# Kernel tuning notes

Hardware: AMD Instinct MI355X
Metric: run time of the kernel (lower is better)

## Reference

```python
import jax, jax.numpy as jnp
import numpy as np

B, S, HID = 2, 2048, 2048
NH, NKV, HD = 16, 4, 128  # num_heads, num_kv_heads, head_dim; kqv_size = NH*HD = 2048
KV_DIM = NKV * HD  # 512


def setup_inputs() -> dict:
    key = jax.random.key(0)
    ks = jax.random.split(key, 7)
    sc = 0.02
    return {
        "hidden_states": jax.random.normal(ks[0], (B, S, HID), dtype=jnp.float32),
        "Wq": jax.random.normal(ks[1], (NH * HD, HID), dtype=jnp.float32) * sc,
        "Wk": jax.random.normal(ks[2], (KV_DIM, HID), dtype=jnp.float32) * sc,
        "Wv": jax.random.normal(ks[3], (KV_DIM, HID), dtype=jnp.float32) * sc,
        "Wo": jax.random.normal(ks[4], (HID, NH * HD), dtype=jnp.float32) * sc,
        "bo": jnp.zeros((HID,), dtype=jnp.float32),
    }


def reference(hidden_states, Wq, Wk, Wv, Wo, bo):
    b, s, _ = hidden_states.shape
    # projections (nn.Linear: x @ W.T), no bias on q/k/v
    q = (hidden_states @ Wq.T).reshape(b, s, NH, HD).transpose(0, 2, 1, 3)   # [B,NH,S,HD]
    k = (hidden_states @ Wk.T).reshape(b, s, NKV, HD).transpose(0, 2, 1, 3)  # [B,NKV,S,HD]
    v = (hidden_states @ Wv.T).reshape(b, s, NKV, HD).transpose(0, 2, 1, 3)
    # GQA: query head h uses kv head h // (NH // NKV)
    g = NH // NKV
    k_rep = jnp.repeat(k, g, axis=1)  # [B,NH,S,HD]
    v_rep = jnp.repeat(v, g, axis=1)
    # float32 upcast, NO 1/sqrt(d) scaling (GPT-Neo style)
    qf = q.astype(jnp.float32)
    kf = k_rep.astype(jnp.float32)
    scores = jnp.einsum("bhqd,bhkd->bhqk", qf, kf)  # [B,NH,S,S]
    causal = jnp.tril(jnp.ones((s, s), dtype=bool))[None, None]
    neg = jnp.finfo(scores.dtype).min
    scores = jnp.where(causal, scores, neg)
    attn = jax.nn.softmax(scores, axis=-1).astype(v.dtype)  # dropout p=0 (eval)
    out = jnp.einsum("bhqk,bhkd->bhqd", attn, v_rep)         # [B,NH,S,HD]
    out = out.transpose(0, 2, 1, 3).reshape(b, s, NH * HD)
    return out @ Wo.T + bo
```

## Files before the change

kernel.cpp:

```cpp
#include <hip/hip_runtime.h>

typedef _Float16 f16;
typedef __attribute__((ext_vector_type(4))) _Float16 f16x4;
typedef __attribute__((ext_vector_type(8))) _Float16 f16x8;
typedef __attribute__((ext_vector_type(4))) float f32x4;

#define NB 2
#define NS 2048
#define NHID 2048
#define N_H 16
#define N_KV 4
#define N_HD 128

__device__ __forceinline__ void gload16(void* lds, const void* g) {
  __builtin_amdgcn_global_load_lds(
      (const __attribute__((address_space(1))) unsigned int*)g,
      (__attribute__((address_space(3))) unsigned int*)lds, 16, 0, 0);
}

__global__ __launch_bounds__(256) void cvt_all(
    const float* __restrict__ hs, const float* __restrict__ Wq,
    const float* __restrict__ Wk, const float* __restrict__ Wv,
    const float* __restrict__ Wo, f16* __restrict__ Xh,
    f16* __restrict__ Wqkv, f16* __restrict__ Woh) {
  int i = blockIdx.x * 256 + threadIdx.x;
  const float* src;
  f16* dst;
  int j;
  if (i < 2097152)      { src = hs; dst = Xh;             j = i; }
  else if (i < 3145728) { src = Wq; dst = Wqkv;           j = i - 2097152; }
  else if (i < 3407872) { src = Wk; dst = Wqkv + 4194304; j = i - 3145728; }
  else if (i < 3670016) { src = Wv; dst = Wqkv + 5242880; j = i - 3407872; }
  else                  { src = Wo; dst = Woh;            j = i - 3670016; }
  const float4 v = reinterpret_cast<const float4*>(src)[j];
  f16x4 o = {(f16)v.x, (f16)v.y, (f16)v.z, (f16)v.w};
  reinterpret_cast<f16x4*>(dst)[j] = o;
}

__global__ __launch_bounds__(512, 2) void gemm_qkv(
    const f16* __restrict__ A, const f16* __restrict__ Bm,
    f16* __restrict__ q_out, f16* __restrict__ k_out, f16* __restrict__ vt_out) {
  constexpr int K = 2048;
  constexpr int NT = 32;
  __shared__ f16 lds[2][28672];
  const int t = threadIdx.x;
  const int l = t & 63, w = t >> 6;
  const int g = l >> 4, l15 = l & 15;
  const int wr = w >> 2, wc = w & 3;
  const int orig = blockIdx.x;
  const int x = orig & 7, loc = orig >> 3;
  const int mb = (x & 3) * 4 + (loc & 3);
  const int nb = (x >> 2) * 8 + (loc >> 2);
  const f16* Ab = A + (size_t)(mb * 256) * K;
  const f16* Bb = Bm + (size_t)(nb * 192) * K;

  const int rr = ((t >> 5) << 3) | (t & 7);
  const int cc = (t >> 3) & 3;
  const int dstw = w * 512;
  int srcB[3];
#pragma unroll
  for (int j = 0; j < 3; ++j) {
    int db0 = j * 4096 + t * 8;
    int h = (db0 >= 6144) ? 1 : 0;
    int u = (db0 - h * 6144) >> 3;
    int rowB = ((u >> 5) << 3) | (u & 7);
    int ccB = (u >> 3) & 3;
    srcB[j] = rowB * K + h * 32 + ccB * 8;
  }

  auto stageA = [&](int tile, int j) {
    int h = j >> 1, gi = j & 1;
    gload16(&lds[tile & 1][h * 8192 + gi * 4096 + dstw],
            Ab + (size_t)(gi * 128 + rr) * K + tile * 64 + h * 32 + cc * 8);
  };
  auto stageB = [&](int tile, int j) {
    gload16(&lds[tile & 1][16384 + j * 4096 + dstw],
            Bb + (size_t)srcB[j] + tile * 64);
  };

  const int fragoff = ((l15 >> 3) << 8) + (g << 6) + ((l15 & 7) << 3);
  f32x4 acc[8][3] = {};

#pragma unroll
  for (int j = 0; j < 3; ++j) stageB(0, j);
#pragma unroll
  for (int j = 0; j < 4; ++j) stageA(0, j);
#pragma unroll
  for (int j = 0; j < 3; ++j) stageB(1, j);
  asm volatile("s_waitcnt vmcnt(3)" ::: "memory");
  __builtin_amdgcn_s_barrier();

  f16x8 bf[3][2];
  for (int T = 0; T < NT; ++T) {
    const f16* buf = lds[T & 1];
#pragma unroll
    for (int q = 0; q < 4; ++q) {
      f16x8 af[2][2];
#pragma unroll
      for (int i = 0; i < 2; ++i)
#pragma unroll
        for (int ks = 0; ks < 2; ++ks)
          af[i][ks] = *reinterpret_cast<const f16x8*>(
              buf + ks * 8192 + (wr * 128 + (2 * q + i) * 16) * 32 + fragoff);
      if (q == 0) {
#pragma unroll
        for (int ni = 0; ni < 3; ++ni)
#pragma unroll
          for (int ks = 0; ks < 2; ++ks)
            bf[ni][ks] = *reinterpret_cast<const f16x8*>(
                buf + 16384 + ks * 6144 + (wc * 48 + ni * 16) * 32 + fragoff);
      }
      if (q == 0)      { if (T + 1 < NT) { stageA(T + 1, 0); stageA(T + 1, 1); } }
      else if (q == 1) { if (T + 1 < NT) { stageA(T + 1, 2); stageA(T + 1, 3); } }
      else if (q == 2) { if (T + 2 < NT) { stageB(T + 2, 0); stageB(T + 2, 1); } }
      else             { if (T + 2 < NT) { stageB(T + 2, 2); } }
      __builtin_amdgcn_s_barrier();
      asm volatile("s_waitcnt lgkmcnt(0)" ::: "memory");
      __builtin_amdgcn_sched_barrier(0);
      __builtin_amdgcn_s_setprio(1);
#pragma unroll
      for (int i = 0; i < 2; ++i)
#pragma unroll
        for (int ni = 0; ni < 3; ++ni)
#pragma unroll
          for (int ks = 0; ks < 2; ++ks)
            acc[2 * q + i][ni] = __builtin_amdgcn_mfma_f32_16x16x32_f16(
                af[i][ks], bf[ni][ks], acc[2 * q + i][ni], 0, 0, 0);
      __builtin_amdgcn_s_setprio(0);
      if (q == 3 && T + 1 < NT) {
        if (T + 2 < NT) asm volatile("s_waitcnt vmcnt(3)" ::: "memory");
        else            asm volatile("s_waitcnt vmcnt(0)" ::: "memory");
      }
      __builtin_amdgcn_s_barrier();
    }
  }

#pragma unroll
  for (int mi = 0; mi < 8; ++mi) {
    int m0 = mb * 256 + wr * 128 + mi * 16 + 4 * g;
    int b = m0 >> 11, s0 = m0 & (NS - 1);
#pragma unroll
    for (int ni = 0; ni < 3; ++ni) {
      int n = nb * 192 + wc * 48 + ni * 16 + l15;
      if (n < 2048) {
        int h = n >> 7, d = n & 127;
        f16* qp = q_out + (((size_t)(b * N_H + h)) * NS + s0) * N_HD + d;
#pragma unroll
        for (int r = 0; r < 4; ++r) qp[r * N_HD] = (f16)acc[mi][ni][r];
      } else if (n < 2560) {
        int n2 = n - 2048, kvh = n2 >> 7, d = n2 & 127;
        f16* kp = k_out + (((size_t)(b * N_KV + kvh)) * NS + s0) * N_HD + d;
#pragma unroll
        for (int r = 0; r < 4; ++r) kp[r * N_HD] = (f16)acc[mi][ni][r];
      } else {
        int n3 = n - 2560, kvh = n3 >> 7, d = n3 & 127;
        f16x4 o4 = {(f16)acc[mi][ni][0], (f16)acc[mi][ni][1],
                    (f16)acc[mi][ni][2], (f16)acc[mi][ni][3]};
        *reinterpret_cast<f16x4*>(
            vt_out + (((size_t)(b * N_KV + kvh)) * N_HD + d) * NS + s0) = o4;
      }
    }
  }
}

__global__ __launch_bounds__(512, 2) void gemm_out(
    const f16* __restrict__ A, const f16* __restrict__ Bm,
    float* __restrict__ f_out, const float* __restrict__ bias) {
  constexpr int K = 2048;
  constexpr int NT = 32;
  __shared__ f16 lds[2][24576];
  const int t = threadIdx.x;
  const int l = t & 63, w = t >> 6;
  const int g = l >> 4, l15 = l & 15;
  const int wr = w >> 2, wc = w & 3;
  const int orig = blockIdx.x;
  const int x = orig & 7, loc = orig >> 3;
  const int mb = (x & 3) * 8 + (loc & 7);
  const int nb = (x >> 2) * 4 + (loc >> 3);
  const f16* Ab = A + (size_t)(mb * 128) * K;
  const f16* Bb = Bm + (size_t)(nb * 256) * K;

  const int rr = ((t >> 5) << 3) | (t & 7);
  const int cc = (t >> 3) & 3;
  const int dstw = w * 512;

  auto stageA = [&](int tile, int h) {
    gload16(&lds[tile & 1][h * 4096 + dstw],
            Ab + (size_t)rr * K + tile * 64 + h * 32 + cc * 8);
  };
  auto stageB = [&](int tile, int j) {
    int h = j >> 1, gi = j & 1;
    gload16(&lds[tile & 1][8192 + h * 8192 + gi * 4096 + dstw],
            Bb + (size_t)(gi * 128 + rr) * K + tile * 64 + h * 32 + cc * 8);
  };

  const int fragoff = ((l15 >> 3) << 8) + (g << 6) + ((l15 & 7) << 3);
  f32x4 acc[4][4] = {};

  stageA(0, 0); stageA(0, 1);
#pragma unroll
  for (int j = 0; j < 4; ++j) stageB(0, j);
#pragma unroll
  for (int j = 0; j < 4; ++j) stageB(1, j);
  asm volatile("s_waitcnt vmcnt(4)" ::: "memory");
  __builtin_amdgcn_s_barrier();

  f16x8 bf[4][2];
  for (int T = 0; T < NT; ++T) {
    const f16* buf = lds[T & 1];
#pragma unroll
    for (int q = 0; q < 2; ++q) {
      f16x8 af[2][2];
#pragma unroll
      for (int i = 0; i < 2; ++i)
#pragma unroll
        for (int ks = 0; ks < 2; ++ks)
          af[i][ks] = *reinterpret_cast<const f16x8*>(
              buf + ks * 4096 + (wr * 64 + (2 * q + i) * 16) * 32 + fragoff);
      if (q == 0) {
#pragma unroll
        for (int ni = 0; ni < 4; ++ni)
#pragma unroll
          for (int ks = 0; ks < 2; ++ks)
            bf[ni][ks] = *reinterpret_cast<const f16x8*>(
                buf + 8192 + ks * 8192 + (wc * 64 + ni * 16) * 32 + fragoff);
      }
      if (q == 0) {
        if (T + 1 < NT) { stageA(T + 1, 0); stageA(T + 1, 1); }
      } else {
        if (T + 2 < NT) { stageB(T + 2, 0); stageB(T + 2, 1); stageB(T + 2, 2); stageB(T + 2, 3); }
      }
      __builtin_amdgcn_s_barrier();
      asm volatile("s_waitcnt lgkmcnt(0)" ::: "memory");
      __builtin_amdgcn_sched_barrier(0);
      __builtin_amdgcn_s_setprio(1);
#pragma unroll
      for (int i = 0; i < 2; ++i)
#pragma unroll
        for (int ni = 0; ni < 4; ++ni)
#pragma unroll
          for (int ks = 0; ks < 2; ++ks)
            acc[2 * q + i][ni] = __builtin_amdgcn_mfma_f32_16x16x32_f16(
                af[i][ks], bf[ni][ks], acc[2 * q + i][ni], 0, 0, 0);
      __builtin_amdgcn_s_setprio(0);
      if (q == 1 && T + 1 < NT) {
        if (T + 2 < NT) asm volatile("s_waitcnt vmcnt(4)" ::: "memory");
        else            asm volatile("s_waitcnt vmcnt(0)" ::: "memory");
      }
      __builtin_amdgcn_s_barrier();
    }
  }

#pragma unroll
  for (int mi = 0; mi < 4; ++mi) {
    int m0 = mb * 128 + wr * 64 + mi * 16 + 4 * g;
#pragma unroll
    for (int ni = 0; ni < 4; ++ni) {
      int n = nb * 256 + wc * 64 + ni * 16 + l15;
#pragma unroll
      for (int r = 0; r < 4; ++r)
        f_out[(size_t)(m0 + r) * NHID + n] = acc[mi][ni][r] + bias[n];
    }
  }
}

__device__ __forceinline__ void stage_kv(const f16* __restrict__ Kp,
                                         const f16* __restrict__ Vp,
                                         f16* Kl, f16* Vl, int kt, int w, int l) {
#pragma unroll
  for (int it = 0; it < 4; ++it) {
    int cb = (it * 4 + w) * 64;
    int c = cb + l;
    int krow = c >> 4, pch = c & 15;
    int sch = (pch & 8) | ((pch ^ krow) & 7);
    gload16(Kl + cb * 8, Kp + (size_t)(kt * 64 + krow) * N_HD + sch * 8);
  }
#pragma unroll
  for (int it = 0; it < 4; ++it) {
    int cb = (it * 4 + w) * 64;
    int c = cb + l;
    int drow = c >> 3, pch = c & 7;
    int sch = (pch ^ drow) & 7;
    gload16(Vl + cb * 8, Vp + (size_t)drow * NS + kt * 64 + sch * 8);
  }
}

__device__ __forceinline__ void attn_step(
    const f16x8* qf, f32x4* oacc, float* mrow, float* lrow, int q0, int kt,
    const f16* Kl, const f16* Vl, f16* Pw, int g, int l15, bool diag) {
  f32x4 sacc[4];
#pragma unroll
  for (int nt = 0; nt < 4; ++nt) {
    f32x4 z = {0.f, 0.f, 0.f, 0.f};
#pragma unroll
    for (int ks = 0; ks < 4; ++ks) {
      int kr = nt * 16 + l15;
      int ch = ks * 4 + g;
      int sw = (ch & 8) | ((ch ^ kr) & 7);
      f16x8 kf = *reinterpret_cast<const f16x8*>(Kl + kr * 128 + sw * 8);
      z = __builtin_amdgcn_mfma_f32_16x16x32_f16(qf[ks], kf, z, 0, 0, 0);
    }
    sacc[nt] = z;
  }

  float p[4][4];
#pragma unroll
  for (int r = 0; r < 4; ++r) {
    int qg = q0 + r;
    float m = -3.0e38f;
#pragma unroll
    for (int nt = 0; nt < 4; ++nt) {
      float sv = sacc[nt][r];
      if (diag) {
        int kg = kt * 64 + nt * 16 + l15;
        if (kg > qg) sv = -3.0e38f;
      }
      p[nt][r] = sv;
      m = fmaxf(m, sv);
    }
#pragma unroll
    for (int off = 8; off >= 1; off >>= 1) m = fmaxf(m, __shfl_xor(m, off));
    float m2 = fmaxf(mrow[r], m);
    float alpha = __builtin_amdgcn_exp2f(mrow[r] - m2);
    mrow[r] = m2;
    lrow[r] *= alpha;
#pragma unroll
    for (int nt = 0; nt < 4; ++nt)
      p[nt][r] = __builtin_amdgcn_exp2f(p[nt][r] - m2);
#pragma unroll
    for (int dt = 0; dt < 8; ++dt) oacc[dt][r] *= alpha;
  }

#pragma unroll
  for (int nt = 0; nt < 4; ++nt)
#pragma unroll
    for (int r = 0; r < 4; ++r) {
      int ql = 4 * g + r;
      int kp = nt * 16 + l15;
      int ch = kp >> 3;
      int idx = ql * 64 + (ch ^ (ql & 7)) * 8 + (kp & 7);
      Pw[idx] = (f16)p[nt][r];
    }
  asm volatile("s_waitcnt lgkmcnt(0)" ::: "memory");
  __builtin_amdgcn_sched_barrier(0);

  f16x8 pa[2];
#pragma unroll
  for (int ks2 = 0; ks2 < 2; ++ks2) {
    int ch = ks2 * 4 + g;
    pa[ks2] = *reinterpret_cast<const f16x8*>(&Pw[l15 * 64 + (ch ^ (l15 & 7)) * 8]);
  }
  const f16x8 ones = {(f16)1.f, (f16)1.f, (f16)1.f, (f16)1.f,
                      (f16)1.f, (f16)1.f, (f16)1.f, (f16)1.f};
  f32x4 lacc = {0.f, 0.f, 0.f, 0.f};
#pragma unroll
  for (int ks2 = 0; ks2 < 2; ++ks2)
    lacc = __builtin_amdgcn_mfma_f32_16x16x32_f16(pa[ks2], ones, lacc, 0, 0, 0);
#pragma unroll
  for (int dt = 0; dt < 8; ++dt)
#pragma unroll
    for (int ks2 = 0; ks2 < 2; ++ks2) {
      int d = dt * 16 + l15;
      int ch = ks2 * 4 + g;
      f16x8 vf = *reinterpret_cast<const f16x8*>(Vl + d * 64 + (ch ^ (d & 7)) * 8);
      oacc[dt] = __builtin_amdgcn_mfma_f32_16x16x32_f16(pa[ks2], vf, oacc[dt], 0, 0, 0);
    }
#pragma unroll
  for (int r = 0; r < 4; ++r) lrow[r] += lacc[r];
}

__global__ __launch_bounds__(256, 2) void attn_kernel(
    const f16* __restrict__ Q, const f16* __restrict__ K,
    const f16* __restrict__ Vt, f16* __restrict__ O) {
  __shared__ f16 Klds[2][64 * 128];
  __shared__ f16 Vlds[2][128 * 64];
  __shared__ f16 Plds[4][16 * 64];
  const int t = threadIdx.x, l = t & 63, w = t >> 6;
  const int g = l >> 4, l15 = l & 15;
  const int orig = blockIdx.x;
  const int x = orig & 7, loc = orig >> 3;
  const int b = x >> 2, kvh = x & 3;
  const int h = kvh * 4 + (loc & 3);
  const int pi = loc >> 2;
  const int qtA = pi, qtB = 31 - pi;
  const f16* Qp = Q + ((size_t)(b * N_H + h)) * NS * N_HD;
  const f16* Kp = K + ((size_t)(b * N_KV + kvh)) * NS * N_HD;
  const f16* Vp = Vt + ((size_t)(b * N_KV + kvh)) * N_HD * NS;

  const f16 l2e = (f16)1.44269504f;
  f16x8 qfA[4], qfB[4];
  const int qrA = qtA * 64 + w * 16 + l15;
  const int qrB = qtB * 64 + w * 16 + l15;
#pragma unroll
  for (int ks = 0; ks < 4; ++ks) {
    qfA[ks] = *reinterpret_cast<const f16x8*>(Qp + (size_t)qrA * N_HD + ks * 32 + g * 8);
    qfB[ks] = *reinterpret_cast<const f16x8*>(Qp + (size_t)qrB * N_HD + ks * 32 + g * 8);
#pragma unroll
    for (int j = 0; j < 8; ++j) { qfA[ks][j] *= l2e; qfB[ks][j] *= l2e; }
  }

  f32x4 oA[8] = {}, oB[8] = {};
  float mA[4], lAr[4], mB[4], lBr[4];
#pragma unroll
  for (int r = 0; r < 4; ++r) {
    mA[r] = -3.0e38f; lAr[r] = 0.f;
    mB[r] = -3.0e38f; lBr[r] = 0.f;
  }
  const int q0A = qtA * 64 + w * 16 + 4 * g;
  const int q0B = qtB * 64 + w * 16 + 4 * g;

  const int nkt = qtB + 1;
  stage_kv(Kp, Vp, Klds[0], Vlds[0], 0, w, l);
  asm volatile("s_waitcnt vmcnt(0)" ::: "memory");
  __syncthreads();
  int cur = 0;
  for (int kt = 0; kt < nkt; ++kt) {
    if (kt + 1 < nkt)
      stage_kv(Kp, Vp, Klds[cur ^ 1], Vlds[cur ^ 1], kt + 1, w, l);
    attn_step(qfB, oB, mB, lBr, q0B, kt, Klds[cur], Vlds[cur], Plds[w], g, l15, kt == qtB);
    if (kt <= qtA)
      attn_step(qfA, oA, mA, lAr, q0A, kt, Klds[cur], Vlds[cur], Plds[w], g, l15, kt == qtA);
    asm volatile("s_waitcnt vmcnt(0)" ::: "memory");
    __syncthreads();
    cur ^= 1;
  }

#pragma unroll
  for (int r = 0; r < 4; ++r) {
    float invB = 1.0f / lBr[r];
    f16* orowB = O + (size_t)(b * NS + q0B + r) * NHID + h * N_HD;
#pragma unroll
    for (int dt = 0; dt < 8; ++dt) orowB[dt * 16 + l15] = (f16)(oB[dt][r] * invB);
    float invA = 1.0f / lAr[r];
    f16* orowA = O + (size_t)(b * NS + q0A + r) * NHID + h * N_HD;
#pragma unroll
    for (int dt = 0; dt < 8; ++dt) orowA[dt * 16 + l15] = (f16)(oA[dt][r] * invA);
  }
}

extern "C" void kernel_launch(void* const* d_in, const int* in_sizes, int n_in,
                              void* d_out, int out_size, void* d_ws, size_t ws_size,
                              hipStream_t stream) {
  const float* hs = (const float*)d_in[0];
  const float* Wq = (const float*)d_in[1];
  const float* Wk = (const float*)d_in[2];
  const float* Wv = (const float*)d_in[3];
  const float* Wo = (const float*)d_in[4];
  const float* bo = (const float*)d_in[5];
  float* out = (float*)d_out;

  char* ws = (char*)d_ws;
  f16* Xh   = (f16*)(ws);
  f16* Wqkv = (f16*)(ws + 16777216);
  f16* Woh  = (f16*)(ws + 29360128);
  f16* Qb   = (f16*)(ws + 37748736);
  f16* Kb   = (f16*)(ws + 54525952);
  f16* Vtb  = (f16*)(ws + 62914560);
  f16* Ob   = Xh;

  cvt_all<<<18432, 256, 0, stream>>>(hs, Wq, Wk, Wv, Wo, Xh, Wqkv, Woh);
  gemm_qkv<<<256, 512, 0, stream>>>(Xh, Wqkv, Qb, Kb, Vtb);
  attn_kernel<<<512, 256, 0, stream>>>(Qb, Kb, Vtb, Ob);
  gemm_out<<<256, 512, 0, stream>>>(Ob, Woh, out, bo);
}
```

Measured before the change: 203.8 us.

## Split paired q-tiles into separate blocks and read V directly from global

The attention kernel no longer pairs two query tiles per block. It launches one block per query tile (1024 blocks), with alternating heads reversing tile order to balance the causal work. V is no longer staged in LDS; each lane loads its V fragments straight from global memory inside the PV loop, and launch bounds rise to 4 blocks per CU to cut LDS and register use. This trades K/V reuse across the two tiles and coalesced LDS-staged V loads for higher occupancy, but exposes global latency on V inside the MFMA loop.

```diff
diff --git a/kernel.cpp b/kernel.cpp
--- a/kernel.cpp
+++ b/kernel.cpp
@@ -264,9 +264,8 @@
   }
 }
 
-__device__ __forceinline__ void stage_kv(const f16* __restrict__ Kp,
-                                         const f16* __restrict__ Vp,
-                                         f16* Kl, f16* Vl, int kt, int w, int l) {
+__device__ __forceinline__ void stage_k(const f16* __restrict__ Kp,
+                                        f16* Kl, int kt, int w, int l) {
 #pragma unroll
   for (int it = 0; it < 4; ++it) {
     int cb = (it * 4 + w) * 64;
@@ -275,19 +274,11 @@
     int sch = (pch & 8) | ((pch ^ krow) & 7);
     gload16(Kl + cb * 8, Kp + (size_t)(kt * 64 + krow) * N_HD + sch * 8);
   }
-#pragma unroll
-  for (int it = 0; it < 4; ++it) {
-    int cb = (it * 4 + w) * 64;
-    int c = cb + l;
-    int drow = c >> 3, pch = c & 7;
-    int sch = (pch ^ drow) & 7;
-    gload16(Vl + cb * 8, Vp + (size_t)drow * NS + kt * 64 + sch * 8);
-  }
 }
 
 __device__ __forceinline__ void attn_step(
     const f16x8* qf, f32x4* oacc, float* mrow, float* lrow, int q0, int kt,
-    const f16* Kl, const f16* Vl, f16* Pw, int g, int l15, bool diag) {
+    const f16* Kl, const f16* __restrict__ Vp, f16* Pw, int g, int l15, bool diag) {
   f32x4 sacc[4];
 #pragma unroll
   for (int nt = 0; nt < 4; ++nt) {
@@ -356,70 +347,62 @@
 #pragma unroll
   for (int ks2 = 0; ks2 < 2; ++ks2)
     lacc = __builtin_amdgcn_mfma_f32_16x16x32_f16(pa[ks2], ones, lacc, 0, 0, 0);
-#pragma unroll
-  for (int dt = 0; dt < 8; ++dt)
+
+  const f16* vbase = Vp + (size_t)kt * 64;
+#pragma unroll
+  for (int dt = 0; dt < 8; ++dt) {
+    const f16* vrow = vbase + (size_t)(dt * 16 + l15) * NS;
 #pragma unroll
     for (int ks2 = 0; ks2 < 2; ++ks2) {
-      int d = dt * 16 + l15;
-      int ch = ks2 * 4 + g;
-      f16x8 vf = *reinterpret_cast<const f16x8*>(Vl + d * 64 + (ch ^ (d & 7)) * 8);
+      f16x8 vf = *reinterpret_cast<const f16x8*>(vrow + ks2 * 32 + g * 8);
       oacc[dt] = __builtin_amdgcn_mfma_f32_16x16x32_f16(pa[ks2], vf, oacc[dt], 0, 0, 0);
     }
+  }
 #pragma unroll
   for (int r = 0; r < 4; ++r) lrow[r] += lacc[r];
 }
 
-__global__ __launch_bounds__(256, 2) void attn_kernel(
+__global__ __launch_bounds__(256, 4) void attn_kernel(
     const f16* __restrict__ Q, const f16* __restrict__ K,
     const f16* __restrict__ Vt, f16* __restrict__ O) {
   __shared__ f16 Klds[2][64 * 128];
-  __shared__ f16 Vlds[2][128 * 64];
   __shared__ f16 Plds[4][16 * 64];
   const int t = threadIdx.x, l = t & 63, w = t >> 6;
   const int g = l >> 4, l15 = l & 15;
   const int orig = blockIdx.x;
   const int x = orig & 7, loc = orig >> 3;
   const int b = x >> 2, kvh = x & 3;
-  const int h = kvh * 4 + (loc & 3);
-  const int pi = loc >> 2;
-  const int qtA = pi, qtB = 31 - pi;
+  const int jj = loc >> 5, c = loc & 31;
+  const int h = kvh * 4 + jj;
+  const int qt = (jj & 1) ? (31 - c) : c;
   const f16* Qp = Q + ((size_t)(b * N_H + h)) * NS * N_HD;
   const f16* Kp = K + ((size_t)(b * N_KV + kvh)) * NS * N_HD;
   const f16* Vp = Vt + ((size_t)(b * N_KV + kvh)) * N_HD * NS;
 
   const f16 l2e = (f16)1.44269504f;
-  f16x8 qfA[4], qfB[4];
-  const int qrA = qtA * 64 + w * 16 + l15;
-  const int qrB = qtB * 64 + w * 16 + l15;
+  f16x8 qf[4];
+  const int qr = qt * 64 + w * 16 + l15;
 #pragma unroll
   for (int ks = 0; ks < 4; ++ks) {
-    qfA[ks] = *reinterpret_cast<const f16x8*>(Qp + (size_t)qrA * N_HD + ks * 32 + g * 8);
-    qfB[ks] = *reinterpret_cast<const f16x8*>(Qp + (size_t)qrB * N_HD + ks * 32 + g * 8);
-#pragma unroll
-    for (int j = 0; j < 8; ++j) { qfA[ks][j] *= l2e; qfB[ks][j] *= l2e; }
-  }
-
-  f32x4 oA[8] = {}, oB[8] = {};
-  float mA[4], lAr[4], mB[4], lBr[4];
-#pragma unroll
-  for (int r = 0; r < 4; ++r) {
-    mA[r] = -3.0e38f; lAr[r] = 0.f;
-    mB[r] = -3.0e38f; lBr[r] = 0.f;
-  }
-  const int q0A = qtA * 64 + w * 16 + 4 * g;
-  const int q0B = qtB * 64 + w * 16 + 4 * g;
-
-  const int nkt = qtB + 1;
-  stage_kv(Kp, Vp, Klds[0], Vlds[0], 0, w, l);
+    qf[ks] = *reinterpret_cast<const f16x8*>(Qp + (size_t)qr * N_HD + ks * 32 + g * 8);
+#pragma unroll
+    for (int j = 0; j < 8; ++j) qf[ks][j] *= l2e;
+  }
+
+  f32x4 o[8] = {};
+  float m[4], lr[4];
+#pragma unroll
+  for (int r = 0; r < 4; ++r) { m[r] = -3.0e38f; lr[r] = 0.f; }
+  const int q0 = qt * 64 + w * 16 + 4 * g;
+
+  stage_k(Kp, Klds[0], 0, w, l);
   asm volatile("s_waitcnt vmcnt(0)" ::: "memory");
   __syncthreads();
   int cur = 0;
-  for (int kt = 0; kt < nkt; ++kt) {
-    if (kt + 1 < nkt)
-      stage_kv(Kp, Vp, Klds[cur ^ 1], Vlds[cur ^ 1], kt + 1, w, l);
-    attn_step(qfB, oB, mB, lBr, q0B, kt, Klds[cur], Vlds[cur], Plds[w], g, l15, kt == qtB);
-    if (kt <= qtA)
-      attn_step(qfA, oA, mA, lAr, q0A, kt, Klds[cur], Vlds[cur], Plds[w], g, l15, kt == qtA);
+  for (int kt = 0; kt <= qt; ++kt) {
+    if (kt < qt)
+      stage_k(Kp, Klds[cur ^ 1], kt + 1, w, l);
+    attn_step(qf, o, m, lr, q0, kt, Klds[cur], Vp, Plds[w], g, l15, kt == qt);
     asm volatile("s_waitcnt vmcnt(0)" ::: "memory");
     __syncthreads();
     cur ^= 1;
@@ -427,14 +410,10 @@
 
 #pragma unroll
   for (int r = 0; r < 4; ++r) {
-    float invB = 1.0f / lBr[r];
-    f16* orowB = O + (size_t)(b * NS + q0B + r) * NHID + h * N_HD;
-#pragma unroll
-    for (int dt = 0; dt < 8; ++dt) orowB[dt * 16 + l15] = (f16)(oB[dt][r] * invB);
-    float invA = 1.0f / lAr[r];
-    f16* orowA = O + (size_t)(b * NS + q0A + r) * NHID + h * N_HD;
-#pragma unroll
-    for (int dt = 0; dt < 8; ++dt) orowA[dt * 16 + l15] = (f16)(oA[dt][r] * invA);
+    float inv = 1.0f / lr[r];
+    f16* orow = O + (size_t)(b * NS + q0 + r) * NHID + h * N_HD;
+#pragma unroll
+    for (int dt = 0; dt < 8; ++dt) orow[dt * 16 + l15] = (f16)(o[dt][r] * inv);
   }
 }
 
@@ -460,6 +439,6 @@
 
   cvt_all<<<18432, 256, 0, stream>>>(hs, Wq, Wk, Wv, Wo, Xh, Wqkv, Woh);
   gemm_qkv<<<256, 512, 0, stream>>>(Xh, Wqkv, Qb, Kb, Vtb);
-  attn_kernel<<<512, 256, 0, stream>>>(Qb, Kb, Vtb, Ob);
+  attn_kernel<<<1024, 256, 0, stream>>>(Qb, Kb, Vtb, Ob);
   gemm_out<<<256, 512, 0, stream>>>(Ob, Woh, out, bo);
 }
```

New measurement: 301.6 us. 1.48x slower.
